# Optimization experiments

Measured on AMD Instinct MI355X. Metric: run time of the kernel, lower is better.

## Reference

```python
import jax, jax.numpy as jnp
import numpy as np
from jax import lax

SEQ_LEN = 256
INPUT_DIM = 1
HIDDEN = 1024
NUM_CLASSES = 10
BATCH = 512


def _kaiming_uniform(key, shape):
    # torch kaiming_uniform_ default: bound = sqrt(6 / fan_in), fan_in = shape[1]
    fan_in = shape[1]
    bound = float(np.sqrt(6.0 / fan_in))
    return jax.random.uniform(key, shape, jnp.float32, -bound, bound)


def setup_inputs() -> dict:
    key = jax.random.key(0)
    ks = jax.random.split(key, 16)
    inp = {"x": jax.random.normal(ks[0], (BATCH, SEQ_LEN), jnp.float32)}
    names_shapes = [
        ("Wgx", (HIDDEN, INPUT_DIM)), ("Wgh", (HIDDEN, HIDDEN)), ("bg", (HIDDEN, 1)),
        ("Wix", (HIDDEN, INPUT_DIM)), ("Wih", (HIDDEN, HIDDEN)), ("bi", (HIDDEN, 1)),
        ("Wfx", (HIDDEN, INPUT_DIM)), ("Wfh", (HIDDEN, HIDDEN)), ("bf", (HIDDEN, 1)),
        ("Wox", (HIDDEN, INPUT_DIM)), ("Woh", (HIDDEN, HIDDEN)), ("bo", (HIDDEN, 1)),
        ("Wph", (NUM_CLASSES, HIDDEN)), ("bp", (NUM_CLASSES, 1)),
    ]
    for k, (name, shape) in zip(ks[1:], names_shapes):
        inp[name] = _kaiming_uniform(k, shape)
    return inp


def reference(x, Wgx, Wgh, bg, Wix, Wih, bi, Wfx, Wfh, bf, Wox, Woh, bo, Wph, bp):
    B = x.shape[0]
    H = Wgh.shape[0]
    h0 = jnp.zeros((H, B), x.dtype)
    c0 = jnp.zeros((H, B), x.dtype)
    xs = x.T  # [S, B]; each step xt is [B] (input_dim == 1)

    def step(carry, xt):
        ht, ct = carry
        xt = xt[None, :]  # [1, B]
        g = jnp.tanh(Wgx @ xt + Wgh @ ht + bg)
        i = jax.nn.sigmoid(Wix @ xt + Wih @ ht + bi)
        f = jax.nn.sigmoid(Wfx @ xt + Wfh @ ht + bf)
        o = jax.nn.sigmoid(Wox @ xt + Woh @ ht + bo)
        ct = g * i + ct * f
        ht = jnp.tanh(ct) * o
        return (ht, ct), None

    (ht, ct), _ = lax.scan(step, (h0, c0), xs)
    pt = Wph @ ht + bp  # [num_classes, B], only last step's pt is returned
    return pt.T  # [B, num_classes]
```

## Files before the change

### kernel.cpp

```cpp
#include <hip/hip_runtime.h>


#define HID  1024
#define SEQL 256

typedef __bf16 bf16x8 __attribute__((ext_vector_type(8)));
typedef float  f32x16 __attribute__((ext_vector_type(16)));
typedef unsigned u32x4 __attribute__((ext_vector_type(4)));

#define AS1 __attribute__((address_space(1)))
#define AS3 __attribute__((address_space(3)))

__device__ __forceinline__ float fast_sigmoid(float v) {
    float e = __expf(-v);
    return 1.0f / (1.0f + e);
}
__device__ __forceinline__ float fast_tanh(float v) {
    float e = __expf(2.0f * v);
    return 1.0f - 2.0f / (e + 1.0f);
}
__device__ __forceinline__ unsigned pk2bf(float a, float b) {
    unsigned short ua = __builtin_bit_cast(unsigned short, (__bf16)a);
    unsigned short ub = __builtin_bit_cast(unsigned short, (__bf16)b);
    return (unsigned)ua | ((unsigned)ub << 16);
}
__device__ __forceinline__ float bfhi(unsigned u) { return __builtin_bit_cast(float, u & 0xFFFF0000u); }
__device__ __forceinline__ float bflo(unsigned u) { return __builtin_bit_cast(float, u << 16); }

__device__ __forceinline__ void store_sc1(unsigned* p, unsigned v) {
    asm volatile("global_store_dword %0, %1, off sc1" :: "v"(p), "v"(v) : "memory");
}
__device__ __forceinline__ u32x4 load16_sc1(const void* p) {
    u32x4 r;
    asm volatile("global_load_dwordx4 %0, %1, off sc1\n\t"
                 "s_waitcnt vmcnt(0)" : "=v"(r) : "v"(p) : "memory");
    return r;
}
__device__ __forceinline__ u32x4 load16_sc0(const void* p) {
    u32x4 r;
    asm volatile("global_load_dwordx4 %0, %1, off sc0\n\t"
                 "s_waitcnt vmcnt(0)" : "=v"(r) : "v"(p) : "memory");
    return r;
}

__global__ __launch_bounds__(256) void lstm_init(unsigned* sync, float* out) {
    int idx = blockIdx.x * 256 + threadIdx.x;
    if (idx < 768) store_sc1(sync + idx, 0u);
    if (idx < 5120) out[idx] = 0.05f;
}

__global__ __attribute__((amdgpu_flat_work_group_size(256, 256), amdgpu_waves_per_eu(1, 1)))
void lstm_main(
    const float* __restrict__ x,
    const float* __restrict__ Wgx, const float* __restrict__ Wgh, const float* __restrict__ bg,
    const float* __restrict__ Wix, const float* __restrict__ Wih, const float* __restrict__ bi,
    const float* __restrict__ Wfx, const float* __restrict__ Wfh, const float* __restrict__ bf_,
    const float* __restrict__ Wox, const float* __restrict__ Woh, const float* __restrict__ bo,
    const float* __restrict__ Wph, const float* __restrict__ bp,
    float* __restrict__ out,
    unsigned short* __restrict__ htA, unsigned short* __restrict__ htB,
    unsigned* __restrict__ sync)
{
    extern __shared__ uint4 ldsB[];

    const int tid = threadIdx.x;
    const int w   = tid >> 6;
    const int l   = tid & 63;
    const int l31 = l & 31;
    const int h5  = l >> 5;
    const int gid = blockIdx.x;
    const int c   = gid & 7;
    const int r   = gid >> 3;

    const int gate = l31 >> 3;
    const int hrow = (r << 5) + (w << 3) + (l & 7);
    const float* Wsel = (gate == 0) ? Wgh : (gate == 1) ? Wih : (gate == 2) ? Wfh : Woh;
    const float* wrow = Wsel + hrow * HID + (h5 << 3);
    bf16x8 A[64];
#pragma unroll
    for (int kk = 0; kk < 64; ++kk) {
        const float4* p = (const float4*)(wrow + kk * 16);
        float4 u0 = p[0], u1 = p[1];
        bf16x8 a;
        a[0] = (__bf16)u0.x; a[1] = (__bf16)u0.y; a[2] = (__bf16)u0.z; a[3] = (__bf16)u0.w;
        a[4] = (__bf16)u1.x; a[5] = (__bf16)u1.y; a[6] = (__bf16)u1.z; a[7] = (__bf16)u1.w;
        A[kk] = a;
        __builtin_amdgcn_sched_barrier(0);
    }

    float wx16[16], bs16[16];
    {
        const float* WxA[4] = {Wgx, Wix, Wfx, Wox};
        const float* bA[4]  = {bg, bi, bf_, bo};
#pragma unroll
        for (int j = 0; j < 16; ++j) {
            int g = j >> 2;
            int h = (r << 5) + (w << 3) + (j & 3) + (h5 << 2);
            wx16[j] = WxA[g][h];
            bs16[j] = bA[g][h];
        }
    }

    unsigned xcd;
    asm volatile("s_getreg_b32 %0, hwreg(HW_REG_XCC_ID)" : "=s"(xcd));
    unsigned* xslot = sync + 512;
    if (tid == 0) store_sc1(xslot + gid, xcd + 1u);
    bool fast;
    {
        const unsigned* sp = xslot + c + (l31 << 3);
        unsigned sv;
        while (true) {
            sv = __hip_atomic_load(sp, __ATOMIC_RELAXED, __HIP_MEMORY_SCOPE_AGENT);
            if (__ballot(sv >= 1u && sv <= 8u) == ~0ull) break;
            __builtin_amdgcn_s_sleep(1);
        }
        fast = (__ballot(sv == xcd + 1u) == ~0ull);
    }

    float ct[8];
#pragma unroll
    for (int i = 0; i < 8; ++i) ct[i] = 0.f;

    const unsigned short* htR = htA;
    unsigned short*       htW = htB;
    unsigned* gflags = sync + (c << 6);
    const float* xrow0 = x + (unsigned)((c << 6) + l31) * SEQL;
    const float* xrow1 = x + (unsigned)((c << 6) + 32 + l31) * SEQL;

    float xv0 = xrow0[0], xv1 = xrow1[0];

    for (int t = 0; t < SEQL; ++t) {
        int tn = (t + 1 < SEQL) ? t + 1 : t;
        float nx0 = xrow0[tn], nx1 = xrow1[tn];

        f32x16 acc0, acc1;
#pragma unroll
        for (int j = 0; j < 16; ++j) {
            acc0[j] = fmaf(wx16[j], xv0, bs16[j]);
            acc1[j] = fmaf(wx16[j], xv1, bs16[j]);
        }

        if (t > 0) {
            const unsigned short* gR = htR + (c << 16);

            if (fast) {
#pragma unroll
                for (int ch = 0; ch < 4; ++ch)
#pragma unroll
                    for (int j = 0; j < 8; ++j) {
                        int q = (w << 3) + j;
                        const void* g = (const void*)(gR + ch * 16384 + q * 512 + (l << 3));
                        __builtin_amdgcn_global_load_lds((const AS1 void*)g,
                            (AS3 void*)&ldsB[(ch * 32 + q) * 64], 16, 0, 0x1 );
                    }
            } else {
#pragma unroll
                for (int ch = 0; ch < 4; ++ch)
#pragma unroll
                    for (int j = 0; j < 8; ++j) {
                        int q = (w << 3) + j;
                        const void* g = (const void*)(gR + ch * 16384 + q * 512 + (l << 3));
                        __builtin_amdgcn_global_load_lds((const AS1 void*)g,
                            (AS3 void*)&ldsB[(ch * 32 + q) * 64], 16, 0, 0x10 );
                    }
            }
            __builtin_amdgcn_sched_barrier(0);

#pragma unroll
            for (int ch = 0; ch < 4; ++ch) {
                if      (ch == 0) asm volatile("s_waitcnt vmcnt(24)" ::: "memory");
                else if (ch == 1) asm volatile("s_waitcnt vmcnt(16)" ::: "memory");
                else if (ch == 2) asm volatile("s_waitcnt vmcnt(8)"  ::: "memory");
                else              asm volatile("s_waitcnt vmcnt(0)"  ::: "memory");
                __builtin_amdgcn_s_barrier();
                asm volatile("" ::: "memory");
#pragma unroll
                for (int kk = 0; kk < 16; ++kk) {
                    bf16x8 b0 = __builtin_bit_cast(bf16x8, ldsB[(ch * 32 + kk * 2 + 0) * 64 + l]);
                    bf16x8 b1 = __builtin_bit_cast(bf16x8, ldsB[(ch * 32 + kk * 2 + 1) * 64 + l]);
                    acc0 = __builtin_amdgcn_mfma_f32_32x32x16_bf16(A[ch * 16 + kk], b0, acc0, 0, 0, 0);
                    acc1 = __builtin_amdgcn_mfma_f32_32x32x16_bf16(A[ch * 16 + kk], b1, acc1, 0, 0, 0);
                }
            }
        }

        float htv[8];
#pragma unroll
        for (int nt = 0; nt < 2; ++nt) {
            f32x16 ac = nt ? acc1 : acc0;
#pragma unroll
            for (int d = 0; d < 4; ++d) {
                float g  = fast_tanh(ac[d]);
                float ii = fast_sigmoid(ac[4 + d]);
                float ff = fast_sigmoid(ac[8 + d]);
                float oo = fast_sigmoid(ac[12 + d]);
                float cc = fmaf(ct[nt * 4 + d], ff, g * ii);
                ct[nt * 4 + d] = cc;
                htv[nt * 4 + d] = fast_tanh(cc) * oo;
            }
        }

        {
            unsigned short* gW = htW + (c << 16);
            int kkw  = (r << 1) + (w >> 1);
            int slot = ((w & 1) << 5) + l31;
#pragma unroll
            for (int nt = 0; nt < 2; ++nt) {
                unsigned lo = pk2bf(htv[nt * 4 + 0], htv[nt * 4 + 1]);
                unsigned hi = pk2bf(htv[nt * 4 + 2], htv[nt * 4 + 3]);
                unsigned long long v = (unsigned long long)lo | ((unsigned long long)hi << 32);
                unsigned long long* dst =
                    (unsigned long long*)(gW + (((kkw * 2 + nt) * 64 + slot) * 8 + (h5 << 2)));
                if (fast) *dst = v;
                else __hip_atomic_store(dst, v, __ATOMIC_RELAXED, __HIP_MEMORY_SCOPE_AGENT);
            }
        }

        asm volatile("s_waitcnt vmcnt(0)" ::: "memory");
        __syncthreads();
        unsigned target = (unsigned)(t + 1);
        if (tid == 0)
            __hip_atomic_store(&gflags[r], target, __ATOMIC_RELAXED, __HIP_MEMORY_SCOPE_AGENT);
        if (w == 0) {
            const unsigned* fp = gflags + l31;
            while (true) {
                unsigned v = __hip_atomic_load(fp, __ATOMIC_RELAXED, __HIP_MEMORY_SCOPE_AGENT);
                if (__ballot(v >= target) == ~0ull) break;
                __builtin_amdgcn_s_sleep(1);
            }
        }
        __syncthreads();

        xv0 = nx0; xv1 = nx1;
        const unsigned short* tmp = htR; htR = htW; htW = (unsigned short*)tmp;
    }

    {
        const unsigned short* hfin = htR + (c << 16);
        for (int p = w; p < 20; p += 4) {
            int bloc = (r << 1) + (p / 10);
            int bb   = (c << 6) + bloc;
            int cls  = p % 10;
            const unsigned short* base = hfin + l * 1024 + ((bloc >> 5) & 1) * 512
                                              + (bloc & 31) * 8;
            u32x4 u0, u1;
            if (fast) { u0 = load16_sc0(base); u1 = load16_sc0(base + 256); }
            else      { u0 = load16_sc1(base); u1 = load16_sc1(base + 256); }
            const float* wp = Wph + (unsigned)cls * HID + (unsigned)l * 16;
            float s = 0.f;
#pragma unroll
            for (int e = 0; e < 4; ++e) {
                s = fmaf(wp[2 * e],         bflo(u0[e]), s);
                s = fmaf(wp[2 * e + 1],     bfhi(u0[e]), s);
                s = fmaf(wp[8 + 2 * e],     bflo(u1[e]), s);
                s = fmaf(wp[8 + 2 * e + 1], bfhi(u1[e]), s);
            }
#pragma unroll
            for (int off = 32; off > 0; off >>= 1) s += __shfl_xor(s, off, 64);
            if (l == 0) out[bb * 10 + cls] = s + bp[cls];
        }
    }
}

extern "C" void kernel_launch(void* const* d_in, const int* in_sizes, int n_in,
                              void* d_out, int out_size, void* d_ws, size_t ws_size,
                              hipStream_t stream) {
    const float* x   = (const float*)d_in[0];
    const float* Wgx = (const float*)d_in[1];
    const float* Wgh = (const float*)d_in[2];
    const float* bg  = (const float*)d_in[3];
    const float* Wix = (const float*)d_in[4];
    const float* Wih = (const float*)d_in[5];
    const float* bi  = (const float*)d_in[6];
    const float* Wfx = (const float*)d_in[7];
    const float* Wfh = (const float*)d_in[8];
    const float* bf_ = (const float*)d_in[9];
    const float* Wox = (const float*)d_in[10];
    const float* Woh = (const float*)d_in[11];
    const float* bo  = (const float*)d_in[12];
    const float* Wph = (const float*)d_in[13];
    const float* bp  = (const float*)d_in[14];
    float* out = (float*)d_out;

    char* ws = (char*)d_ws;
    unsigned short* htA = (unsigned short*)ws;
    unsigned short* htB = (unsigned short*)(ws + (1 << 20));
    unsigned*      sync = (unsigned*)(ws + (2 << 20));

    lstm_init<<<dim3(20), dim3(256), 0, stream>>>(sync, out);

    static int lds_set = 0;
    if (!lds_set) {
        hipFuncSetAttribute((const void*)lstm_main,
                            hipFuncAttributeMaxDynamicSharedMemorySize, 131072);
        lds_set = 1;
    }
    lstm_main<<<dim3(256), dim3(256), 131072, stream>>>(
        x, Wgx, Wgh, bg, Wix, Wih, bi, Wfx, Wfh, bf_,
        Wox, Woh, bo, Wph, bp, out, htA, htB, sync);
}
```

Baseline: 1.764 ms.

## Split K dimension across waves with LDS cross-wave reduction of gate accumulators

Each wave now owns a quarter of the hidden-state K dimension for all four row tiles, instead of a 256-row slice over the full K. The per-chunk block barriers inside the MFMA loop go away, since each wave consumes only its own global-to-LDS loads. The partial sums are then exchanged through LDS and reduced so each wave finishes its own tile before the activations. This adds LDS write and read traffic, one barrier, and eight live accumulators per wave, which raises register pressure.

```diff
diff --git a/kernel.cpp b/kernel.cpp
--- a/kernel.cpp
+++ b/kernel.cpp
@@ -10,6 +10,7 @@
 
 #define AS1 __attribute__((address_space(1)))
 #define AS3 __attribute__((address_space(3)))
+#define MFMA __builtin_amdgcn_mfma_f32_32x32x16_bf16
 
 __device__ __forceinline__ float fast_sigmoid(float v) {
     float e = __expf(-v);
@@ -73,19 +74,21 @@
     const int r   = gid >> 3;
 
     const int gate = l31 >> 3;
-    const int hrow = (r << 5) + (w << 3) + (l & 7);
     const float* Wsel = (gate == 0) ? Wgh : (gate == 1) ? Wih : (gate == 2) ? Wfh : Woh;
-    const float* wrow = Wsel + hrow * HID + (h5 << 3);
     bf16x8 A[64];
 #pragma unroll
-    for (int kk = 0; kk < 64; ++kk) {
-        const float4* p = (const float4*)(wrow + kk * 16);
-        float4 u0 = p[0], u1 = p[1];
-        bf16x8 a;
-        a[0] = (__bf16)u0.x; a[1] = (__bf16)u0.y; a[2] = (__bf16)u0.z; a[3] = (__bf16)u0.w;
-        a[4] = (__bf16)u1.x; a[5] = (__bf16)u1.y; a[6] = (__bf16)u1.z; a[7] = (__bf16)u1.w;
-        A[kk] = a;
-        __builtin_amdgcn_sched_barrier(0);
+    for (int tq = 0; tq < 4; ++tq) {
+#pragma unroll
+        for (int kq = 0; kq < 16; ++kq) {
+            const float* p = Wsel + (unsigned)((r << 5) + (tq << 3) + (l & 7)) * HID
+                                  + (w << 8) + (kq << 4) + (h5 << 3);
+            float4 u0 = ((const float4*)p)[0], u1 = ((const float4*)p)[1];
+            bf16x8 a;
+            a[0] = (__bf16)u0.x; a[1] = (__bf16)u0.y; a[2] = (__bf16)u0.z; a[3] = (__bf16)u0.w;
+            a[4] = (__bf16)u1.x; a[5] = (__bf16)u1.y; a[6] = (__bf16)u1.z; a[7] = (__bf16)u1.w;
+            A[tq * 16 + kq] = a;
+            __builtin_amdgcn_sched_barrier(0);
+        }
     }
 
     float wx16[16], bs16[16];
@@ -117,6 +120,10 @@
         fast = (__ballot(sv == xcd + 1u) == ~0ull);
     }
 
+    f32x16 Z;
+#pragma unroll
+    for (int i = 0; i < 16; ++i) Z[i] = 0.f;
+
     float ct[8];
 #pragma unroll
     for (int i = 0; i < 8; ++i) ct[i] = 0.f;
@@ -126,79 +133,129 @@
     unsigned* gflags = sync + (c << 6);
     const float* xrow0 = x + (unsigned)((c << 6) + l31) * SEQL;
     const float* xrow1 = x + (unsigned)((c << 6) + 32 + l31) * SEQL;
-
     float xv0 = xrow0[0], xv1 = xrow1[0];
+
+#define KSTEP(KQ) do { \
+    uint4 r0 = ldsB[(w << 11) + ((KQ) << 7) + l]; \
+    uint4 r1 = ldsB[(w << 11) + ((KQ) << 7) + 64 + l]; \
+    bf16x8 b0 = __builtin_bit_cast(bf16x8, r0); \
+    bf16x8 b1 = __builtin_bit_cast(bf16x8, r1); \
+    acc00 = MFMA(A[(KQ)],      b0, acc00, 0,0,0); acc01 = MFMA(A[(KQ)],      b1, acc01, 0,0,0); \
+    acc10 = MFMA(A[16 + (KQ)], b0, acc10, 0,0,0); acc11 = MFMA(A[16 + (KQ)], b1, acc11, 0,0,0); \
+    acc20 = MFMA(A[32 + (KQ)], b0, acc20, 0,0,0); acc21 = MFMA(A[32 + (KQ)], b1, acc21, 0,0,0); \
+    acc30 = MFMA(A[48 + (KQ)], b0, acc30, 0,0,0); acc31 = MFMA(A[48 + (KQ)], b1, acc31, 0,0,0); \
+} while (0)
+
+#define PWR4(ACC, POS, NT) do { \
+    int bb = (w << 11) + ((((POS) << 1) + (NT)) << 8) + l; \
+    _Pragma("unroll") for (int j = 0; j < 4; ++j) { \
+        float4 f = {ACC[4*j], ACC[4*j+1], ACC[4*j+2], ACC[4*j+3]}; \
+        ldsB[bb + (j << 6)] = __builtin_bit_cast(uint4, f); } \
+} while (0)
+
+#define PRD4(S, V, POS, NT) do { \
+    int bb = ((V) << 11) + ((((POS) << 1) + (NT)) << 8) + l; \
+    _Pragma("unroll") for (int j = 0; j < 4; ++j) { \
+        float4 f = __builtin_bit_cast(float4, ldsB[bb + (j << 6)]); \
+        S[4*j] += f.x; S[4*j+1] += f.y; S[4*j+2] += f.z; S[4*j+3] += f.w; } \
+} while (0)
+
+#define ACT(S, NT) do { \
+    float xvn = (NT) ? xv1 : xv0; \
+    _Pragma("unroll") for (int d = 0; d < 4; ++d) { \
+        float ag = S[d]      + wx16[d] * xvn      + bs16[d]; \
+        float ai = S[4 + d]  + wx16[4 + d] * xvn  + bs16[4 + d]; \
+        float af = S[8 + d]  + wx16[8 + d] * xvn  + bs16[8 + d]; \
+        float ao = S[12 + d] + wx16[12 + d] * xvn + bs16[12 + d]; \
+        float g = fast_tanh(ag); float ii = fast_sigmoid(ai); \
+        float ff = fast_sigmoid(af); float oo = fast_sigmoid(ao); \
+        float cc = fmaf(ct[(NT) * 4 + d], ff, g * ii); \
+        ct[(NT) * 4 + d] = cc; \
+        htv[(NT) * 4 + d] = fast_tanh(cc) * oo; } \
+} while (0)
+
+#define FINW(ACC0, ACC1, V1, P1, V2, P2, V3, P3) do { \
+    float s0[16]; \
+    _Pragma("unroll") for (int j = 0; j < 16; ++j) s0[j] = ACC0[j]; \
+    PRD4(s0, V1, P1, 0); PRD4(s0, V2, P2, 0); PRD4(s0, V3, P3, 0); \
+    ACT(s0, 0); \
+    float s1[16]; \
+    _Pragma("unroll") for (int j = 0; j < 16; ++j) s1[j] = ACC1[j]; \
+    PRD4(s1, V1, P1, 1); PRD4(s1, V2, P2, 1); PRD4(s1, V3, P3, 1); \
+    ACT(s1, 1); \
+} while (0)
 
     for (int t = 0; t < SEQL; ++t) {
         int tn = (t + 1 < SEQL) ? t + 1 : t;
-        float nx0 = xrow0[tn], nx1 = xrow1[tn];
-
-        f32x16 acc0, acc1;
-#pragma unroll
-        for (int j = 0; j < 16; ++j) {
-            acc0[j] = fmaf(wx16[j], xv0, bs16[j]);
-            acc1[j] = fmaf(wx16[j], xv1, bs16[j]);
-        }
+        float nx0, nx1;
+
+        f32x16 acc00 = Z, acc01 = Z, acc10 = Z, acc11 = Z;
+        f32x16 acc20 = Z, acc21 = Z, acc30 = Z, acc31 = Z;
 
         if (t > 0) {
             const unsigned short* gR = htR + (c << 16);
-
             if (fast) {
 #pragma unroll
-                for (int ch = 0; ch < 4; ++ch)
-#pragma unroll
-                    for (int j = 0; j < 8; ++j) {
-                        int q = (w << 3) + j;
-                        const void* g = (const void*)(gR + ch * 16384 + q * 512 + (l << 3));
-                        __builtin_amdgcn_global_load_lds((const AS1 void*)g,
-                            (AS3 void*)&ldsB[(ch * 32 + q) * 64], 16, 0, 0x1 );
-                    }
+                for (int j = 0; j < 32; ++j) {
+                    const void* g = (const void*)(gR + ((w << 5) + j) * 512 + (l << 3));
+                    __builtin_amdgcn_global_load_lds((const AS1 void*)g,
+                        (AS3 void*)&ldsB[(w << 11) + (j << 6)], 16, 0, 0x1 );
+                }
             } else {
 #pragma unroll
-                for (int ch = 0; ch < 4; ++ch)
-#pragma unroll
-                    for (int j = 0; j < 8; ++j) {
-                        int q = (w << 3) + j;
-                        const void* g = (const void*)(gR + ch * 16384 + q * 512 + (l << 3));
-                        __builtin_amdgcn_global_load_lds((const AS1 void*)g,
-                            (AS3 void*)&ldsB[(ch * 32 + q) * 64], 16, 0, 0x10 );
-                    }
-            }
-            __builtin_amdgcn_sched_barrier(0);
-
-#pragma unroll
-            for (int ch = 0; ch < 4; ++ch) {
-                if      (ch == 0) asm volatile("s_waitcnt vmcnt(24)" ::: "memory");
-                else if (ch == 1) asm volatile("s_waitcnt vmcnt(16)" ::: "memory");
-                else if (ch == 2) asm volatile("s_waitcnt vmcnt(8)"  ::: "memory");
-                else              asm volatile("s_waitcnt vmcnt(0)"  ::: "memory");
-                __builtin_amdgcn_s_barrier();
-                asm volatile("" ::: "memory");
-#pragma unroll
-                for (int kk = 0; kk < 16; ++kk) {
-                    bf16x8 b0 = __builtin_bit_cast(bf16x8, ldsB[(ch * 32 + kk * 2 + 0) * 64 + l]);
-                    bf16x8 b1 = __builtin_bit_cast(bf16x8, ldsB[(ch * 32 + kk * 2 + 1) * 64 + l]);
-                    acc0 = __builtin_amdgcn_mfma_f32_32x32x16_bf16(A[ch * 16 + kk], b0, acc0, 0, 0, 0);
-                    acc1 = __builtin_amdgcn_mfma_f32_32x32x16_bf16(A[ch * 16 + kk], b1, acc1, 0, 0, 0);
+                for (int j = 0; j < 32; ++j) {
+                    const void* g = (const void*)(gR + ((w << 5) + j) * 512 + (l << 3));
+                    __builtin_amdgcn_global_load_lds((const AS1 void*)g,
+                        (AS3 void*)&ldsB[(w << 11) + (j << 6)], 16, 0, 0x10 );
                 }
             }
-        }
+            __builtin_amdgcn_sched_barrier(0);
+            nx0 = xrow0[tn]; nx1 = xrow1[tn];
+            __builtin_amdgcn_sched_barrier(0);
+
+            asm volatile("s_waitcnt vmcnt(26)" ::: "memory");
+            __builtin_amdgcn_sched_barrier(0);
+            KSTEP(0); KSTEP(1); KSTEP(2); KSTEP(3);
+            asm volatile("s_waitcnt vmcnt(18)" ::: "memory");
+            __builtin_amdgcn_sched_barrier(0);
+            KSTEP(4); KSTEP(5); KSTEP(6); KSTEP(7);
+            asm volatile("s_waitcnt vmcnt(10)" ::: "memory");
+            __builtin_amdgcn_sched_barrier(0);
+            KSTEP(8); KSTEP(9); KSTEP(10); KSTEP(11);
+            asm volatile("s_waitcnt vmcnt(2)" ::: "memory");
+            __builtin_amdgcn_sched_barrier(0);
+            KSTEP(12); KSTEP(13); KSTEP(14); KSTEP(15);
+        } else {
+            nx0 = xrow0[tn]; nx1 = xrow1[tn];
+        }
+
+        if (w == 0) {
+            PWR4(acc10, 0, 0); PWR4(acc11, 0, 1);
+            PWR4(acc20, 1, 0); PWR4(acc21, 1, 1);
+            PWR4(acc30, 2, 0); PWR4(acc31, 2, 1);
+        } else if (w == 1) {
+            PWR4(acc00, 0, 0); PWR4(acc01, 0, 1);
+            PWR4(acc20, 1, 0); PWR4(acc21, 1, 1);
+            PWR4(acc30, 2, 0); PWR4(acc31, 2, 1);
+        } else if (w == 2) {
+            PWR4(acc00, 0, 0); PWR4(acc01, 0, 1);
+            PWR4(acc10, 1, 0); PWR4(acc11, 1, 1);
+            PWR4(acc30, 2, 0); PWR4(acc31, 2, 1);
+        } else {
+            PWR4(acc00, 0, 0); PWR4(acc01, 0, 1);
+            PWR4(acc10, 1, 0); PWR4(acc11, 1, 1);
+            PWR4(acc20, 2, 0); PWR4(acc21, 2, 1);
+        }
+        asm volatile("s_waitcnt lgkmcnt(0)" ::: "memory");
+        __builtin_amdgcn_s_barrier();
+        asm volatile("" ::: "memory");
+        __builtin_amdgcn_sched_barrier(0);
 
         float htv[8];
-#pragma unroll
-        for (int nt = 0; nt < 2; ++nt) {
-            f32x16 ac = nt ? acc1 : acc0;
-#pragma unroll
-            for (int d = 0; d < 4; ++d) {
-                float g  = fast_tanh(ac[d]);
-                float ii = fast_sigmoid(ac[4 + d]);
-                float ff = fast_sigmoid(ac[8 + d]);
-                float oo = fast_sigmoid(ac[12 + d]);
-                float cc = fmaf(ct[nt * 4 + d], ff, g * ii);
-                ct[nt * 4 + d] = cc;
-                htv[nt * 4 + d] = fast_tanh(cc) * oo;
-            }
-        }
+        if (w == 0)      FINW(acc00, acc01, 1, 0, 2, 0, 3, 0);
+        else if (w == 1) FINW(acc10, acc11, 0, 0, 2, 1, 3, 1);
+        else if (w == 2) FINW(acc20, acc21, 0, 1, 1, 1, 3, 2);
+        else             FINW(acc30, acc31, 0, 2, 1, 2, 2, 2);
 
         {
             unsigned short* gW = htW + (c << 16);
```

Result: slower. 3.120 ms (+76.9%).

## Use per-wave flags with all-wave polling and finer-grained LDS load pipelining

Applied to the files above, without the earlier changes.

Replaces the per-block flag and the two __syncthreads around the inter-block barrier with one flag per wave. Every wave polls all 128 flags of its group directly through 64-bit loads, which removes the block-level barriers from the per-timestep critical path. The h-state staging is also reordered into 8 smaller chunks with finer vmcnt waits, so MFMA work can start earlier. The next-x prefetch is moved after the async loads are issued. In exchange, every wave spins on global memory, which adds polling traffic, and the sync area grows.

```diff
diff --git a/kernel.cpp b/kernel.cpp
--- a/kernel.cpp
+++ b/kernel.cpp
@@ -45,7 +45,7 @@
 
 __global__ __launch_bounds__(256) void lstm_init(unsigned* sync, float* out) {
     int idx = blockIdx.x * 256 + threadIdx.x;
-    if (idx < 768) store_sc1(sync + idx, 0u);
+    if (idx < 1280) store_sc1(sync + idx, 0u);
     if (idx < 5120) out[idx] = 0.05f;
 }
 
@@ -103,7 +103,7 @@
 
     unsigned xcd;
     asm volatile("s_getreg_b32 %0, hwreg(HW_REG_XCC_ID)" : "=s"(xcd));
-    unsigned* xslot = sync + 512;
+    unsigned* xslot = sync + 1024;
     if (tid == 0) store_sc1(xslot + gid, xcd + 1u);
     bool fast;
     {
@@ -123,7 +123,9 @@
 
     const unsigned short* htR = htA;
     unsigned short*       htW = htB;
-    unsigned* gflags = sync + (c << 6);
+    unsigned* gflags = sync + (c << 7);
+    unsigned* myflag = gflags + (r << 2) + w;
+    const unsigned long long* pollp = (const unsigned long long*)gflags + l;
     const float* xrow0 = x + (unsigned)((c << 6) + l31) * SEQL;
     const float* xrow1 = x + (unsigned)((c << 6) + 32 + l31) * SEQL;
 
@@ -131,7 +133,7 @@
 
     for (int t = 0; t < SEQL; ++t) {
         int tn = (t + 1 < SEQL) ? t + 1 : t;
-        float nx0 = xrow0[tn], nx1 = xrow1[tn];
+        float nx0, nx1;
 
         f32x16 acc0, acc1;
 #pragma unroll
@@ -145,43 +147,54 @@
 
             if (fast) {
 #pragma unroll
-                for (int ch = 0; ch < 4; ++ch)
-#pragma unroll
-                    for (int j = 0; j < 8; ++j) {
-                        int q = (w << 3) + j;
-                        const void* g = (const void*)(gR + ch * 16384 + q * 512 + (l << 3));
+                for (int ch = 0; ch < 8; ++ch)
+#pragma unroll
+                    for (int j = 0; j < 4; ++j) {
+                        int q = (ch << 4) + (w << 2) + j;
+                        const void* g = (const void*)(gR + q * 512 + (l << 3));
                         __builtin_amdgcn_global_load_lds((const AS1 void*)g,
-                            (AS3 void*)&ldsB[(ch * 32 + q) * 64], 16, 0, 0x1 );
+                            (AS3 void*)&ldsB[q * 64], 16, 0, 0x1 );
                     }
             } else {
 #pragma unroll
-                for (int ch = 0; ch < 4; ++ch)
-#pragma unroll
-                    for (int j = 0; j < 8; ++j) {
-                        int q = (w << 3) + j;
-                        const void* g = (const void*)(gR + ch * 16384 + q * 512 + (l << 3));
+                for (int ch = 0; ch < 8; ++ch)
+#pragma unroll
+                    for (int j = 0; j < 4; ++j) {
+                        int q = (ch << 4) + (w << 2) + j;
+                        const void* g = (const void*)(gR + q * 512 + (l << 3));
                         __builtin_amdgcn_global_load_lds((const AS1 void*)g,
-                            (AS3 void*)&ldsB[(ch * 32 + q) * 64], 16, 0, 0x10 );
+                            (AS3 void*)&ldsB[q * 64], 16, 0, 0x10 );
                     }
             }
             __builtin_amdgcn_sched_barrier(0);
-
-#pragma unroll
-            for (int ch = 0; ch < 4; ++ch) {
-                if      (ch == 0) asm volatile("s_waitcnt vmcnt(24)" ::: "memory");
-                else if (ch == 1) asm volatile("s_waitcnt vmcnt(16)" ::: "memory");
-                else if (ch == 2) asm volatile("s_waitcnt vmcnt(8)"  ::: "memory");
-                else              asm volatile("s_waitcnt vmcnt(0)"  ::: "memory");
+            nx0 = xrow0[tn]; nx1 = xrow1[tn];
+            __builtin_amdgcn_sched_barrier(0);
+
+#pragma unroll
+            for (int ch = 0; ch < 8; ++ch) {
+                switch (ch) {
+                    case 0: asm volatile("s_waitcnt vmcnt(28)" ::: "memory"); break;
+                    case 1: asm volatile("s_waitcnt vmcnt(24)" ::: "memory"); break;
+                    case 2: asm volatile("s_waitcnt vmcnt(20)" ::: "memory"); break;
+                    case 3: asm volatile("s_waitcnt vmcnt(16)" ::: "memory"); break;
+                    case 4: asm volatile("s_waitcnt vmcnt(12)" ::: "memory"); break;
+                    case 5: asm volatile("s_waitcnt vmcnt(8)"  ::: "memory"); break;
+                    case 6: asm volatile("s_waitcnt vmcnt(4)"  ::: "memory"); break;
+                    default: asm volatile("s_waitcnt vmcnt(0)" ::: "memory"); break;
+                }
                 __builtin_amdgcn_s_barrier();
                 asm volatile("" ::: "memory");
 #pragma unroll
-                for (int kk = 0; kk < 16; ++kk) {
-                    bf16x8 b0 = __builtin_bit_cast(bf16x8, ldsB[(ch * 32 + kk * 2 + 0) * 64 + l]);
-                    bf16x8 b1 = __builtin_bit_cast(bf16x8, ldsB[(ch * 32 + kk * 2 + 1) * 64 + l]);
-                    acc0 = __builtin_amdgcn_mfma_f32_32x32x16_bf16(A[ch * 16 + kk], b0, acc0, 0, 0, 0);
-                    acc1 = __builtin_amdgcn_mfma_f32_32x32x16_bf16(A[ch * 16 + kk], b1, acc1, 0, 0, 0);
+                for (int k2 = 0; k2 < 8; ++k2) {
+                    int kk = (ch << 3) + k2;
+                    bf16x8 b0 = __builtin_bit_cast(bf16x8, ldsB[(kk * 2 + 0) * 64 + l]);
+                    bf16x8 b1 = __builtin_bit_cast(bf16x8, ldsB[(kk * 2 + 1) * 64 + l]);
+                    acc0 = __builtin_amdgcn_mfma_f32_32x32x16_bf16(A[kk], b0, acc0, 0, 0, 0);
+                    acc1 = __builtin_amdgcn_mfma_f32_32x32x16_bf16(A[kk], b1, acc1, 0, 0, 0);
                 }
             }
+        } else {
+            nx0 = xrow0[tn]; nx1 = xrow1[tn];
         }
 
         float htv[8];
@@ -217,19 +230,16 @@
         }
 
         asm volatile("s_waitcnt vmcnt(0)" ::: "memory");
-        __syncthreads();
         unsigned target = (unsigned)(t + 1);
-        if (tid == 0)
-            __hip_atomic_store(&gflags[r], target, __ATOMIC_RELAXED, __HIP_MEMORY_SCOPE_AGENT);
-        if (w == 0) {
-            const unsigned* fp = gflags + l31;
-            while (true) {
-                unsigned v = __hip_atomic_load(fp, __ATOMIC_RELAXED, __HIP_MEMORY_SCOPE_AGENT);
-                if (__ballot(v >= target) == ~0ull) break;
-                __builtin_amdgcn_s_sleep(1);
-            }
-        }
-        __syncthreads();
+        if (l == 0)
+            __hip_atomic_store(myflag, target, __ATOMIC_RELAXED, __HIP_MEMORY_SCOPE_AGENT);
+        while (true) {
+            unsigned long long v = __hip_atomic_load(pollp, __ATOMIC_RELAXED,
+                                                     __HIP_MEMORY_SCOPE_AGENT);
+            if (__ballot(((unsigned)v >= target) && ((unsigned)(v >> 32) >= target)) == ~0ull)
+                break;
+            __builtin_amdgcn_s_sleep(1);
+        }
 
         xv0 = nx0; xv1 = nx1;
         const unsigned short* tmp = htR; htR = htW; htW = (unsigned short*)tmp;
```

New measurement: 4.013 ms. 128% more time.

## Replace global per-step barrier with per-chunk flag gating overlapped with MFMA

Applied to the files above, without the earlier changes.

Removes the end-of-step wait for all 32 row-groups. Each of the four K-chunks of the hidden state is now gated only on the 8 producer flags that write it, so staging and MFMA on early chunks can start before later producers finish. The next chunk's flags are prefetched into LDS through global_load_lds, with a spin poll as the fallback when they are not yet set. This adds flag traffic and LDS space. With double buffering it also risks a producer overwriting a buffer that a slow consumer is still reading.

```diff
diff --git a/kernel.cpp b/kernel.cpp
--- a/kernel.cpp
+++ b/kernel.cpp
@@ -41,6 +41,19 @@
     asm volatile("global_load_dwordx4 %0, %1, off sc0\n\t"
                  "s_waitcnt vmcnt(0)" : "=v"(r) : "v"(p) : "memory");
     return r;
+}
+
+__device__ __forceinline__ void spinpoll8(const unsigned* gflags, int cg, int r,
+                                          unsigned tgt, int l) {
+    const unsigned* fp = gflags + ((cg << 3) + (l & 7));
+    const bool self = (((cg << 3) + (l & 7)) == r);
+    while (true) {
+        unsigned v;
+        asm volatile("global_load_dword %0, %1, off sc1\n\ts_waitcnt vmcnt(0)"
+                     : "=v"(v) : "v"(fp) : "memory");
+        if (__ballot(self || (v >= tgt)) == ~0ull) return;
+        __builtin_amdgcn_s_sleep(1);
+    }
 }
 
 __global__ __launch_bounds__(256) void lstm_init(unsigned* sync, float* out) {
@@ -62,6 +75,7 @@
     unsigned* __restrict__ sync)
 {
     extern __shared__ uint4 ldsB[];
+    unsigned* fl_lds = (unsigned*)((char*)ldsB + 131072);
 
     const int tid = threadIdx.x;
     const int w   = tid >> 6;
@@ -126,8 +140,54 @@
     unsigned* gflags = sync + (c << 6);
     const float* xrow0 = x + (unsigned)((c << 6) + l31) * SEQL;
     const float* xrow1 = x + (unsigned)((c << 6) + 32 + l31) * SEQL;
-
     float xv0 = xrow0[0], xv1 = xrow1[0];
+
+#define STAGE(CH) do { \
+    if (fast) { \
+        _Pragma("unroll") for (int j_ = 0; j_ < 8; ++j_) { \
+            int q_ = (w << 3) + j_; \
+            const void* gsrc_ = (const void*)(gR + (CH) * 16384 + q_ * 512 + (l << 3)); \
+            __builtin_amdgcn_global_load_lds((const AS1 void*)gsrc_, \
+                (AS3 void*)&ldsB[((CH) * 32 + q_) * 64], 16, 0, 0x1 ); \
+        } \
+    } else { \
+        _Pragma("unroll") for (int j_ = 0; j_ < 8; ++j_) { \
+            int q_ = (w << 3) + j_; \
+            const void* gsrc_ = (const void*)(gR + (CH) * 16384 + q_ * 512 + (l << 3)); \
+            __builtin_amdgcn_global_load_lds((const AS1 void*)gsrc_, \
+                (AS3 void*)&ldsB[((CH) * 32 + q_) * 64], 16, 0, 0x10 ); \
+        } \
+    } \
+} while (0)
+
+#define PISSUE(CH) do { if (w == 0) { \
+    const void* fsrc_ = (const void*)(gflags + (((CH) << 3) + (l & 7))); \
+    __builtin_amdgcn_global_load_lds((const AS1 void*)fsrc_, (AS3 void*)fl_lds, 4, 0, 0x10); \
+} } while (0)
+
+#define GATE(CH) do { \
+    if (w == 0) { \
+        asm volatile("s_waitcnt vmcnt(0)" ::: "memory"); \
+        __builtin_amdgcn_sched_barrier(0); \
+        unsigned v_ = fl_lds[l]; \
+        int f_ = ((CH) << 3) + (l & 7); \
+        if (__ballot((f_ == r) || (v_ >= tgt)) != ~0ull) \
+            spinpoll8(gflags, (CH), r, tgt, l); \
+    } else { \
+        asm volatile("s_waitcnt vmcnt(0)" ::: "memory"); \
+        __builtin_amdgcn_sched_barrier(0); \
+    } \
+    __builtin_amdgcn_s_barrier(); \
+    asm volatile("" ::: "memory"); \
+} while (0)
+
+#define MFMACH(CH) \
+    _Pragma("unroll") for (int k2_ = 0; k2_ < 16; ++k2_) { \
+        bf16x8 b0_ = __builtin_bit_cast(bf16x8, ldsB[((CH) * 32 + k2_ * 2 + 0) * 64 + l]); \
+        bf16x8 b1_ = __builtin_bit_cast(bf16x8, ldsB[((CH) * 32 + k2_ * 2 + 1) * 64 + l]); \
+        acc0 = __builtin_amdgcn_mfma_f32_32x32x16_bf16(A[(CH) * 16 + k2_], b0_, acc0, 0, 0, 0); \
+        acc1 = __builtin_amdgcn_mfma_f32_32x32x16_bf16(A[(CH) * 16 + k2_], b1_, acc1, 0, 0, 0); \
+    }
 
     for (int t = 0; t < SEQL; ++t) {
         int tn = (t + 1 < SEQL) ? t + 1 : t;
@@ -142,46 +202,28 @@
 
         if (t > 0) {
             const unsigned short* gR = htR + (c << 16);
-
-            if (fast) {
-#pragma unroll
-                for (int ch = 0; ch < 4; ++ch)
-#pragma unroll
-                    for (int j = 0; j < 8; ++j) {
-                        int q = (w << 3) + j;
-                        const void* g = (const void*)(gR + ch * 16384 + q * 512 + (l << 3));
-                        __builtin_amdgcn_global_load_lds((const AS1 void*)g,
-                            (AS3 void*)&ldsB[(ch * 32 + q) * 64], 16, 0, 0x1 );
-                    }
-            } else {
-#pragma unroll
-                for (int ch = 0; ch < 4; ++ch)
-#pragma unroll
-                    for (int j = 0; j < 8; ++j) {
-                        int q = (w << 3) + j;
-                        const void* g = (const void*)(gR + ch * 16384 + q * 512 + (l << 3));
-                        __builtin_amdgcn_global_load_lds((const AS1 void*)g,
-                            (AS3 void*)&ldsB[(ch * 32 + q) * 64], 16, 0, 0x10 );
-                    }
-            }
-            __builtin_amdgcn_sched_barrier(0);
-
-#pragma unroll
-            for (int ch = 0; ch < 4; ++ch) {
-                if      (ch == 0) asm volatile("s_waitcnt vmcnt(24)" ::: "memory");
-                else if (ch == 1) asm volatile("s_waitcnt vmcnt(16)" ::: "memory");
-                else if (ch == 2) asm volatile("s_waitcnt vmcnt(8)"  ::: "memory");
-                else              asm volatile("s_waitcnt vmcnt(0)"  ::: "memory");
-                __builtin_amdgcn_s_barrier();
-                asm volatile("" ::: "memory");
-#pragma unroll
-                for (int kk = 0; kk < 16; ++kk) {
-                    bf16x8 b0 = __builtin_bit_cast(bf16x8, ldsB[(ch * 32 + kk * 2 + 0) * 64 + l]);
-                    bf16x8 b1 = __builtin_bit_cast(bf16x8, ldsB[(ch * 32 + kk * 2 + 1) * 64 + l]);
-                    acc0 = __builtin_amdgcn_mfma_f32_32x32x16_bf16(A[ch * 16 + kk], b0, acc0, 0, 0, 0);
-                    acc1 = __builtin_amdgcn_mfma_f32_32x32x16_bf16(A[ch * 16 + kk], b1, acc1, 0, 0, 0);
-                }
-            }
+            unsigned tgt = (unsigned)t;
+
+            if (w == 0) spinpoll8(gflags, 0, r, tgt, l);
+            __builtin_amdgcn_s_barrier();
+            asm volatile("" ::: "memory");
+            STAGE(0);
+            PISSUE(1);
+            GATE(1);
+            STAGE(1);
+            PISSUE(2);
+            MFMACH(0);
+            GATE(2);
+            STAGE(2);
+            PISSUE(3);
+            MFMACH(1);
+            GATE(3);
+            STAGE(3);
+            MFMACH(2);
+            asm volatile("s_waitcnt vmcnt(0)" ::: "memory");
+            __builtin_amdgcn_s_barrier();
+            asm volatile("" ::: "memory");
+            MFMACH(3);
         }
 
         float htv[8];
@@ -218,22 +260,25 @@
 
         asm volatile("s_waitcnt vmcnt(0)" ::: "memory");
         __syncthreads();
-        unsigned target = (unsigned)(t + 1);
         if (tid == 0)
-            __hip_atomic_store(&gflags[r], target, __ATOMIC_RELAXED, __HIP_MEMORY_SCOPE_AGENT);
-        if (w == 0) {
-            const unsigned* fp = gflags + l31;
-            while (true) {
-                unsigned v = __hip_atomic_load(fp, __ATOMIC_RELAXED, __HIP_MEMORY_SCOPE_AGENT);
-                if (__ballot(v >= target) == ~0ull) break;
-                __builtin_amdgcn_s_sleep(1);
-            }
-        }
-        __syncthreads();
+            __hip_atomic_store(&gflags[r], (unsigned)(t + 1),
+                               __ATOMIC_RELAXED, __HIP_MEMORY_SCOPE_AGENT);
 
         xv0 = nx0; xv1 = nx1;
         const unsigned short* tmp = htR; htR = htW; htW = (unsigned short*)tmp;
     }
+
+    if (w == 0) {
+        const unsigned* fp = gflags + l31;
+        while (true) {
+            unsigned v;
+            asm volatile("global_load_dword %0, %1, off sc1\n\ts_waitcnt vmcnt(0)"
+                         : "=v"(v) : "v"(fp) : "memory");
+            if (__ballot(v >= (unsigned)SEQL) == ~0ull) break;
+            __builtin_amdgcn_s_sleep(1);
+        }
+    }
+    __syncthreads();
 
     {
         const unsigned short* hfin = htR + (c << 16);
@@ -292,10 +337,10 @@
     static int lds_set = 0;
     if (!lds_set) {
         hipFuncSetAttribute((const void*)lstm_main,
-                            hipFuncAttributeMaxDynamicSharedMemorySize, 131072);
+                            hipFuncAttributeMaxDynamicSharedMemorySize, 131584);
         lds_set = 1;
     }
-    lstm_main<<<dim3(256), dim3(256), 131072, stream>>>(
+    lstm_main<<<dim3(256), dim3(256), 131584, stream>>>(
         x, Wgx, Wgh, bg, Wix, Wih, bi, Wfx, Wfh, bf_,
         Wox, Woh, bo, Wph, bp, out, htA, htB, sync);
 }
```

New measurement: 2.167 ms. 22.9% more time.
